# Kernel optimization log

Hardware: AMD Instinct MI355X
Metric: run time of the kernel (lower is better)

The kernel has to match this reference:

```python
import jax, jax.numpy as jnp
import numpy as np

TEMPERATURE = 0.1
MAX_POS = 6
MAX_NEG = 30
POS_NEG_RATIO = 1.0
NEG_K = max(6, MAX_NEG)  # static top-k width for negatives


def setup_inputs() -> dict:
    key = jax.random.key(0)
    k1, k2 = jax.random.split(key)
    K, D = 8192, 256
    features = jax.random.normal(k1, (K, D), dtype=jnp.float32)
    labels = jax.random.randint(k2, (K,), 0, 64, dtype=jnp.int64)
    return {"features": features, "labels": labels}


def reference(features, labels):
    K = features.shape[0]
    # L2-normalize embeddings (F.normalize, dim=1)
    f = features / jnp.clip(jnp.linalg.norm(features, axis=1, keepdims=True), 1e-12)
    sim = jnp.matmul(f, f.T) / TEMPERATURE                      # [K, K]
    sim = sim - jax.lax.stop_gradient(jnp.max(sim, axis=1, keepdims=True))
    exp_sim = jnp.exp(sim)

    eye = jnp.eye(K, dtype=bool)
    same = labels[:, None] == labels[None, :]
    mask_pos = same & ~eye                                      # same label, off-diagonal
    mask_neg = ~same                                            # 1 - mask_pos - eye

    n_pos = jnp.sum(mask_pos, axis=1).astype(jnp.int32)         # [K]
    n_neg = jnp.sum(mask_neg, axis=1).astype(jnp.int32)         # [K]

    # per-anchor dynamic sample counts (vectorized version of the python loop)
    max_pos_i = jnp.minimum(
        n_pos,
        jnp.maximum(1, jnp.minimum(MAX_POS, (n_neg.astype(jnp.float32) * POS_NEG_RATIO).astype(jnp.int32))),
    )
    max_neg_i = jnp.minimum(n_neg, NEG_K)
    valid_row = (n_pos > 0) & (n_neg > 0)
    max_pos_i = jnp.where(valid_row, max_pos_i, 0)
    max_neg_i = jnp.where(valid_row, max_neg_i, 0)

    rows = jnp.arange(K)[:, None]
    neg_inf = jnp.finfo(sim.dtype).min

    # top-k hard positives by similarity, masked to the first max_pos_i ranks
    pos_scores = jnp.where(mask_pos, sim, neg_inf)
    _, pos_idx = jax.lax.top_k(pos_scores, MAX_POS)             # [K, MAX_POS]
    pos_keep = (jnp.arange(MAX_POS)[None, :] < max_pos_i[:, None]).astype(sim.dtype)
    new_mask_pos = jnp.zeros((K, K), sim.dtype).at[rows, pos_idx].add(pos_keep)

    # random negatives: randperm emulated by top-k of uniform scores over neg slots
    rand = jax.random.uniform(jax.random.key(42), (K, K), dtype=jnp.float32)
    neg_scores = jnp.where(mask_neg, rand, -1.0)
    _, neg_idx = jax.lax.top_k(neg_scores, NEG_K)               # [K, NEG_K]
    neg_keep = (jnp.arange(NEG_K)[None, :] < max_neg_i[:, None]).astype(sim.dtype)
    new_mask_neg = jnp.zeros((K, K), sim.dtype).at[rows, neg_idx].add(neg_keep)

    numerator = jnp.sum(exp_sim * new_mask_pos, axis=1)
    denominator = jnp.sum(exp_sim * (new_mask_pos + new_mask_neg), axis=1)
    loss = -jnp.log(jnp.clip(numerator / denominator, 1e-8))
    return jnp.mean(loss)
```

## Files before the change

kernel.cpp:

```cpp
#include <hip/hip_runtime.h>
#include <hip/hip_fp16.h>
#include <math.h>
#include <stdint.h>


#define NEGK 30
#define MAXP 6
#define MAXBC 320
#define RGB 32
#define CGB 64

typedef _Float16 h2v __attribute__((ext_vector_type(2)));

__device__ __forceinline__ uint64_t mix64(uint64_t z) {
  z += 0x9E3779B97F4A7C15ULL;
  z = (z ^ (z >> 30)) * 0xBF58476D1CE4E5B9ULL;
  z = (z ^ (z >> 27)) * 0x94D049BB133111EBULL;
  return z ^ (z >> 31);
}

__device__ __forceinline__ float wave_reduce_add(float p) {
#pragma unroll
  for (int o = 32; o; o >>= 1) p += __shfl_down(p, o, 64);
  return p;
}

__device__ __forceinline__ float dot8h(uint4 a, uint4 b, float acc) {
  const h2v* pa = (const h2v*)&a;
  const h2v* pb = (const h2v*)&b;
#if __has_builtin(__builtin_amdgcn_fdot2)
#pragma unroll
  for (int q = 0; q < 4; ++q) acc = __builtin_amdgcn_fdot2(pa[q], pb[q], acc, false);
#else
#pragma unroll
  for (int q = 0; q < 4; ++q)
    acc += (float)pa[q].x * (float)pb[q].x + (float)pa[q].y * (float)pb[q].y;
#endif
  return acc;
}

__global__ __launch_bounds__(256) void k_prep(const float* __restrict__ F,
                                              const int* __restrict__ labels, int K,
                                              __half* __restrict__ Fh,
                                              int* __restrict__ g_start,
                                              int* __restrict__ g_soff,
                                              int* __restrict__ g_bucket,
                                              int4* __restrict__ g_meta) {
  __shared__ int cnt[64], start[65], cur[64], soff_s[64];
  const int tid = threadIdx.x;

  if ((int)blockIdx.x < K / 4) {
    const int row = blockIdx.x * 4 + (tid >> 6);
    const int lane = tid & 63;
    const float4 a = ((const float4*)(F + (size_t)row * 256))[lane];
    float p = a.x * a.x + a.y * a.y + a.z * a.z + a.w * a.w;
    p = wave_reduce_add(p);
    p = __shfl(p, 0, 64);
    const float inv = 1.0f / fmaxf(sqrtf(p), 1e-12f);
    union { __half2 h[2]; uint2 u; } cv;
    cv.h[0] = __float22half2_rn(make_float2(a.x * inv, a.y * inv));
    cv.h[1] = __float22half2_rn(make_float2(a.z * inv, a.w * inv));
    ((uint2*)(Fh + (size_t)row * 256))[lane] = cv.u;
    return;
  }

  if (tid < 64) cnt[tid] = 0;
  __syncthreads();
  for (int t = tid; t < K; t += 256) atomicAdd(&cnt[labels[t] & 63], 1);
  __syncthreads();
  if (tid == 0) {
    int acc = 0, sacc = 0;
    for (int l = 0; l < 64; ++l) {
      start[l] = acc;
      const int B = cnt[l];
      acc += B;
      soff_s[l] = sacc;
      const int Bc = B < MAXBC ? B : MAXBC;
      sacc += Bc * Bc;
    }
    start[64] = acc;
  }
  __syncthreads();
  if (tid < 64) { cur[tid] = start[tid]; g_soff[tid] = soff_s[tid]; }
  if (tid < 65) g_start[tid] = start[tid];
  __syncthreads();
  for (int t = tid; t < K; t += 256) {
    const int l = labels[t] & 63;
    const int p = atomicAdd(&cur[l], 1);
    g_bucket[p] = t;
    g_meta[t] = make_int4(start[l], cnt[l], p - start[l], soff_s[l]);
  }
}

__global__ __launch_bounds__(256) void k_gram(const __half* __restrict__ Fh,
                                              const int* __restrict__ g_start,
                                              const int* __restrict__ g_soff,
                                              const int* __restrict__ g_bucket,
                                              float* __restrict__ g_sims) {
  __shared__ uint4 sA[RGB * 32];

  const int b  = blockIdx.x;
  const int bs = g_start[b];
  const int B  = g_start[b + 1] - bs;
  const int Bc = B < MAXBC ? B : MAXBC;
  const int r0 = blockIdx.y * RGB;
  const int c0 = blockIdx.z * CGB;
  if (r0 >= Bc || c0 >= Bc) return;
  const int tid = threadIdx.x;

  for (int u = tid; u < RGB * 32; u += 256) {
    const int r = u >> 5, c = u & 31;
    const int rr = r0 + r;
    const int gr = g_bucket[bs + (rr < Bc ? rr : Bc - 1)];
    sA[u] = ((const uint4*)(Fh + (size_t)gr * 256))[c];
  }
  __syncthreads();

  const int wv = tid >> 6, lane = tid & 63;
  const int cc = c0 + lane;
  const int gq = g_bucket[bs + (cc < Bc ? cc : Bc - 1)];
  const uint4* fq = (const uint4*)(Fh + (size_t)gq * 256);
  const uint4* sw = sA + wv * 8 * 32;

  float acc[8];
#pragma unroll
  for (int r = 0; r < 8; ++r) acc[r] = 0.0f;

  for (int k = 0; k < 32; k += 4) {
    const uint4 a0 = fq[k], a1 = fq[k + 1], a2 = fq[k + 2], a3 = fq[k + 3];
#pragma unroll
    for (int r = 0; r < 8; ++r) {
      float t = acc[r];
      t = dot8h(sw[r * 32 + k    ], a0, t);
      t = dot8h(sw[r * 32 + k + 1], a1, t);
      t = dot8h(sw[r * 32 + k + 2], a2, t);
      t = dot8h(sw[r * 32 + k + 3], a3, t);
      acc[r] = t;
    }
  }

  if (cc < Bc) {
    float* outb = g_sims + g_soff[b];
#pragma unroll
    for (int r = 0; r < 8; ++r) {
      const int rr = r0 + wv * 8 + r;
      if (rr < Bc)
        outb[(size_t)rr * Bc + cc] = (rr == cc) ? -3.0e38f : acc[r] * 10.0f;
    }
  }
}

__global__ __launch_bounds__(256) void k_anchor(
    const __half* __restrict__ Fh, const int* __restrict__ g_bucket,
    const int4* __restrict__ g_meta, const float* __restrict__ g_sims,
    float* __restrict__ g_part, int K) {
  const int wv = threadIdx.x >> 6;
  const int lane = threadIdx.x & 63;
  const int i = blockIdx.x * 4 + wv;

  const int4 mt = g_meta[i];
  const int bs = mt.x, B = mt.y;
  const int Bc = B < MAXBC ? B : MAXBC;
  int loc = mt.z;
  if (loc >= Bc) loc = 0;
  const int n_pos = B - 1;
  const int n_neg = K - B;
  const float* simrow = g_sims + mt.w + (size_t)loc * Bc;

  const int s = lane & 3, g = lane >> 2;
  const uint4* fi4 = (const uint4*)(Fh + (size_t)i * 256);
  uint4 fi[8];
#pragma unroll
  for (int k = 0; k < 8; ++k) fi[k] = fi4[k * 4 + s];

  float v[5];
#pragma unroll
  for (int rr = 0; rr < 5; ++rr) {
    const int t = lane + rr * 64;
    v[rr] = (t < Bc) ? simrow[t] : -3.4e38f;
  }

  int t6 = n_neg < MAXP ? n_neg : MAXP;
  if (t6 < 1) t6 = 1;
  int take = n_pos < t6 ? n_pos : t6;
  if (n_pos <= 0 || n_neg <= 0) take = 0;

  float num = 0.0f;
  for (int r = 0; r < take; ++r) {
    float best = -3.4e38f;
    int bi = 0x7FFFFFFF;
#pragma unroll
    for (int rr = 0; rr < 5; ++rr) {
      if (v[rr] > best) { best = v[rr]; bi = rr * 64 + lane; }
    }
#pragma unroll
    for (int o = 1; o < 64; o <<= 1) {
      const float ov = __shfl_xor(best, o, 64);
      const int oi = __shfl_xor(bi, o, 64);
      if (ov > best || (ov == best && oi < bi)) { best = ov; bi = oi; }
    }
    num += expf(best);
    const int rsel = bi >> 6;
    if ((bi & 63) == lane) {
#pragma unroll
      for (int rr = 0; rr < 5; ++rr)
        if (rr == rsel) v[rr] = -3.4e38f;
    }
  }

  const int target = (take > 0) ? (n_neg < NEGK ? n_neg : NEGK) : 0;
  unsigned int rdraw = 0x40000000u + lane;
  if (lane < target) {
    const uint64_t z = mix64(((uint64_t)(uint32_t)i << 32) | (uint32_t)lane);
    rdraw = (unsigned int)(((uint64_t)(uint32_t)z * (uint64_t)n_neg) >> 32);
  }
  for (int round = 0; round < 8; ++round) {
    bool dup = false;
    for (int l2 = 0; l2 < NEGK; ++l2) {
      const unsigned int vv = __shfl(rdraw, l2, 64);
      if (l2 < lane && vv == rdraw) dup = true;
    }
    if (!__any(dup)) break;
    if (dup && lane < target) {
      const uint64_t z =
          mix64(((uint64_t)(uint32_t)i << 32) | (uint32_t)(lane + 64 * (round + 1)));
      rdraw = (unsigned int)(((uint64_t)(uint32_t)z * (uint64_t)n_neg) >> 32);
    }
  }
  int myj = 0;
  if (lane < target) {
    const int pos = (rdraw < (unsigned int)bs) ? (int)rdraw : (int)rdraw + B;
    myj = g_bucket[pos];
  }

  float e = 0.0f;
#pragma unroll
  for (int r = 0; r < 2; ++r) {
    const int t = r * 16 + g;
    const int j = __shfl(myj, t, 64);
    const uint4* fj = (const uint4*)(Fh + (size_t)j * 256);
    float d = 0.0f;
#pragma unroll
    for (int k = 0; k < 8; ++k) d = dot8h(fj[k * 4 + s], fi[k], d);
    d += __shfl_xor(d, 1, 64);
    d += __shfl_xor(d, 2, 64);
    if (s == 0 && t < target) e += expf(d * 10.0f);
  }
  const float wsum = wave_reduce_add(e);

  if (lane == 0) {
    const float denom = num + wsum;
    float ratio = denom > 0.0f ? num / denom : 0.0f;
    ratio = fmaxf(ratio, 1e-8f);
    g_part[i] = -logf(ratio);
  }
}

__global__ __launch_bounds__(1024) void k_final(const float* __restrict__ g_part,
                                                float* __restrict__ out, int K) {
  __shared__ float s[16];
  float p = 0.0f;
  for (int t = threadIdx.x; t < K; t += 1024) p += g_part[t];
  p = wave_reduce_add(p);
  if ((threadIdx.x & 63) == 0) s[threadIdx.x >> 6] = p;
  __syncthreads();
  if (threadIdx.x == 0) {
    float tot = 0.0f;
#pragma unroll
    for (int w = 0; w < 16; ++w) tot += s[w];
    out[0] = tot / (float)K;
  }
}

extern "C" void kernel_launch(void* const* d_in, const int* in_sizes, int n_in,
                              void* d_out, int out_size, void* d_ws, size_t ws_size,
                              hipStream_t stream) {
  (void)n_in; (void)out_size; (void)ws_size;
  const float* F = (const float*)d_in[0];
  const int* labels = (const int*)d_in[1];
  const int K = in_sizes[1];
  float* out = (float*)d_out;

  char* ws = (char*)d_ws;
  size_t off = 0;
  int*   g_start  = (int*)(ws + off);   off += 512;
  int*   g_soff   = (int*)(ws + off);   off += 256;
  int*   g_bucket = (int*)(ws + off);   off += (size_t)K * 4;
  float* g_part   = (float*)(ws + off); off += (size_t)K * 4;
  off = (off + 255) & ~(size_t)255;
  int4*  g_meta   = (int4*)(ws + off);  off += (size_t)K * 16;
  __half* Fh      = (__half*)(ws + off); off += (size_t)K * 256 * 2;
  float* g_sims   = (float*)(ws + off);  off += (size_t)MAXBC * K * 4;

  k_prep<<<K / 4 + 1, 256, 0, stream>>>(F, labels, K, Fh, g_start, g_soff,
                                        g_bucket, g_meta);
  {
    dim3 grid(64, (MAXBC + RGB - 1) / RGB, (MAXBC + CGB - 1) / CGB);
    k_gram<<<grid, 256, 0, stream>>>(Fh, g_start, g_soff, g_bucket, g_sims);
  }
  k_anchor<<<K / 4, 256, 0, stream>>>(Fh, g_bucket, g_meta, g_sims, g_part, K);
  k_final<<<1, 1024, 0, stream>>>(g_part, out, K);
}
```

Measured before the change: 121.8 us.

## Fuse gram and anchor kernels, keep similarity tiles in registers

Merges the per-label gram kernel and the per-anchor loss kernel into one kernel, so each block computes a 32-anchor by full-bucket similarity tile in registers and does the positive top-k selection and negative sampling directly. This removes the global similarity buffer write and read-back and one kernel launch. The duplicate-rejection loop for negative draws is dropped, so repeated negative indices are no longer resampled. Parallelism drops to 64x10 blocks, each doing the whole row sweep, which risks lower occupancy and more serial work per block.

Measured after the change: 149.9 us. 23.0% more time.

```diff
diff --git a/kernel.cpp b/kernel.cpp
--- a/kernel.cpp
+++ b/kernel.cpp
@@ -7,8 +7,8 @@
 #define NEGK 30
 #define MAXP 6
 #define MAXBC 320
-#define RGB 32
-#define CGB 64
+#define RGM 32
+#define GRIDY ((MAXBC + RGM - 1) / RGM)
 
 typedef _Float16 h2v __attribute__((ext_vector_type(2)));
 
@@ -43,10 +43,8 @@
                                               const int* __restrict__ labels, int K,
                                               __half* __restrict__ Fh,
                                               int* __restrict__ g_start,
-                                              int* __restrict__ g_soff,
-                                              int* __restrict__ g_bucket,
-                                              int4* __restrict__ g_meta) {
-  __shared__ int cnt[64], start[65], cur[64], soff_s[64];
+                                              int* __restrict__ g_bucket) {
+  __shared__ int cnt[64], start[65], cur[64];
   const int tid = threadIdx.x;
 
   if ((int)blockIdx.x < K / 4) {
@@ -69,207 +67,179 @@
   for (int t = tid; t < K; t += 256) atomicAdd(&cnt[labels[t] & 63], 1);
   __syncthreads();
   if (tid == 0) {
-    int acc = 0, sacc = 0;
-    for (int l = 0; l < 64; ++l) {
-      start[l] = acc;
-      const int B = cnt[l];
-      acc += B;
-      soff_s[l] = sacc;
-      const int Bc = B < MAXBC ? B : MAXBC;
-      sacc += Bc * Bc;
-    }
+    int acc = 0;
+    for (int l = 0; l < 64; ++l) { start[l] = acc; acc += cnt[l]; }
     start[64] = acc;
   }
   __syncthreads();
-  if (tid < 64) { cur[tid] = start[tid]; g_soff[tid] = soff_s[tid]; }
+  if (tid < 64) cur[tid] = start[tid];
   if (tid < 65) g_start[tid] = start[tid];
   __syncthreads();
   for (int t = tid; t < K; t += 256) {
     const int l = labels[t] & 63;
     const int p = atomicAdd(&cur[l], 1);
     g_bucket[p] = t;
-    g_meta[t] = make_int4(start[l], cnt[l], p - start[l], soff_s[l]);
-  }
-}
-
-__global__ __launch_bounds__(256) void k_gram(const __half* __restrict__ Fh,
-                                              const int* __restrict__ g_start,
-                                              const int* __restrict__ g_soff,
-                                              const int* __restrict__ g_bucket,
-                                              float* __restrict__ g_sims) {
-  __shared__ uint4 sA[RGB * 32];
+  }
+}
+
+__global__ __launch_bounds__(256) void k_main(
+    const __half* __restrict__ Fh, const int* __restrict__ g_start,
+    const int* __restrict__ g_bucket, float* __restrict__ g_part, int K) {
+  __shared__ uint4 sAnch[RGM * 32];
+  __shared__ int   s_gid[RGM];
+  __shared__ float s_wsum[RGM];
+  __shared__ float s_loss[4];
 
   const int b  = blockIdx.x;
+  const int rg = blockIdx.y;
+  const int bid = b * GRIDY + rg;
   const int bs = g_start[b];
   const int B  = g_start[b + 1] - bs;
   const int Bc = B < MAXBC ? B : MAXBC;
-  const int r0 = blockIdx.y * RGB;
-  const int c0 = blockIdx.z * CGB;
-  if (r0 >= Bc || c0 >= Bc) return;
+  const int p0 = rg * RGM;
   const int tid = threadIdx.x;
-
-  for (int u = tid; u < RGB * 32; u += 256) {
-    const int r = u >> 5, c = u & 31;
-    const int rr = r0 + r;
-    const int gr = g_bucket[bs + (rr < Bc ? rr : Bc - 1)];
-    sA[u] = ((const uint4*)(Fh + (size_t)gr * 256))[c];
-  }
-  __syncthreads();
+  if (p0 >= Bc) { if (tid == 0) g_part[bid] = 0.0f; return; }
 
   const int wv = tid >> 6, lane = tid & 63;
-  const int cc = c0 + lane;
-  const int gq = g_bucket[bs + (cc < Bc ? cc : Bc - 1)];
-  const uint4* fq = (const uint4*)(Fh + (size_t)gq * 256);
-  const uint4* sw = sA + wv * 8 * 32;
-
-  float acc[8];
-#pragma unroll
-  for (int r = 0; r < 8; ++r) acc[r] = 0.0f;
-
-  for (int k = 0; k < 32; k += 4) {
-    const uint4 a0 = fq[k], a1 = fq[k + 1], a2 = fq[k + 2], a3 = fq[k + 3];
-#pragma unroll
-    for (int r = 0; r < 8; ++r) {
-      float t = acc[r];
-      t = dot8h(sw[r * 32 + k    ], a0, t);
-      t = dot8h(sw[r * 32 + k + 1], a1, t);
-      t = dot8h(sw[r * 32 + k + 2], a2, t);
-      t = dot8h(sw[r * 32 + k + 3], a3, t);
-      acc[r] = t;
-    }
-  }
-
-  if (cc < Bc) {
-    float* outb = g_sims + g_soff[b];
-#pragma unroll
-    for (int r = 0; r < 8; ++r) {
-      const int rr = r0 + wv * 8 + r;
-      if (rr < Bc)
-        outb[(size_t)rr * Bc + cc] = (rr == cc) ? -3.0e38f : acc[r] * 10.0f;
-    }
-  }
-}
-
-__global__ __launch_bounds__(256) void k_anchor(
-    const __half* __restrict__ Fh, const int* __restrict__ g_bucket,
-    const int4* __restrict__ g_meta, const float* __restrict__ g_sims,
-    float* __restrict__ g_part, int K) {
-  const int wv = threadIdx.x >> 6;
-  const int lane = threadIdx.x & 63;
-  const int i = blockIdx.x * 4 + wv;
-
-  const int4 mt = g_meta[i];
-  const int bs = mt.x, B = mt.y;
-  const int Bc = B < MAXBC ? B : MAXBC;
-  int loc = mt.z;
-  if (loc >= Bc) loc = 0;
   const int n_pos = B - 1;
   const int n_neg = K - B;
-  const float* simrow = g_sims + mt.w + (size_t)loc * Bc;
-
-  const int s = lane & 3, g = lane >> 2;
-  const uint4* fi4 = (const uint4*)(Fh + (size_t)i * 256);
-  uint4 fi[8];
-#pragma unroll
-  for (int k = 0; k < 8; ++k) fi[k] = fi4[k * 4 + s];
-
-  float v[5];
-#pragma unroll
-  for (int rr = 0; rr < 5; ++rr) {
-    const int t = lane + rr * 64;
-    v[rr] = (t < Bc) ? simrow[t] : -3.4e38f;
+
+  for (int u = tid; u < RGM * 32; u += 256) {
+    const int r = u >> 5, c = u & 31;
+    const int p = p0 + r;
+    const int gr = g_bucket[bs + (p < Bc ? p : Bc - 1)];
+    sAnch[u] = ((const uint4*)(Fh + (size_t)gr * 256))[c];
+  }
+  if (tid < RGM) {
+    const int p = p0 + tid;
+    s_gid[tid] = (p < Bc) ? g_bucket[bs + p] : 0;
+    s_wsum[tid] = 0.0f;
+  }
+  __syncthreads();
+
+  const uint4* sw = sAnch + (wv * 8) * 32;
+
+  float v[5][8];
+#pragma unroll
+  for (int c = 0; c < 5; ++c)
+#pragma unroll
+    for (int r = 0; r < 8; ++r) v[c][r] = -3.4e38f;
+
+#pragma unroll
+  for (int c = 0; c < 5; ++c) {
+    if (c * 64 < Bc) {
+      const int cc = c * 64 + lane;
+      const int gq = g_bucket[bs + (cc < Bc ? cc : Bc - 1)];
+      const uint4* fq = (const uint4*)(Fh + (size_t)gq * 256);
+      float acc[8];
+#pragma unroll
+      for (int r = 0; r < 8; ++r) acc[r] = 0.0f;
+      for (int k = 0; k < 32; k += 4) {
+        const uint4 a0 = fq[k], a1 = fq[k + 1], a2 = fq[k + 2], a3 = fq[k + 3];
+#pragma unroll
+        for (int r = 0; r < 8; ++r) {
+          float t = acc[r];
+          t = dot8h(sw[r * 32 + k    ], a0, t);
+          t = dot8h(sw[r * 32 + k + 1], a1, t);
+          t = dot8h(sw[r * 32 + k + 2], a2, t);
+          t = dot8h(sw[r * 32 + k + 3], a3, t);
+          acc[r] = t;
+        }
+      }
+      if (cc < Bc) {
+#pragma unroll
+        for (int r = 0; r < 8; ++r) {
+          const int p = p0 + wv * 8 + r;
+          v[c][r] = (cc == p) ? -3.0e38f : acc[r] * 10.0f;
+        }
+      }
+    }
   }
 
   int t6 = n_neg < MAXP ? n_neg : MAXP;
   if (t6 < 1) t6 = 1;
   int take = n_pos < t6 ? n_pos : t6;
   if (n_pos <= 0 || n_neg <= 0) take = 0;
-
-  float num = 0.0f;
-  for (int r = 0; r < take; ++r) {
-    float best = -3.4e38f;
-    int bi = 0x7FFFFFFF;
-#pragma unroll
-    for (int rr = 0; rr < 5; ++rr) {
-      if (v[rr] > best) { best = v[rr]; bi = rr * 64 + lane; }
+  const int target = (take > 0) ? (n_neg < NEGK ? n_neg : NEGK) : 0;
+
+  float num[8];
+#pragma unroll
+  for (int r = 0; r < 8; ++r) {
+    float nm = 0.0f;
+    for (int t = 0; t < take; ++t) {
+      float best = -3.4e38f;
+      int bi = 0x7FFFFFFF;
+#pragma unroll
+      for (int c = 0; c < 5; ++c) {
+        if (v[c][r] > best) { best = v[c][r]; bi = c * 64 + lane; }
+      }
+#pragma unroll
+      for (int o = 1; o < 64; o <<= 1) {
+        const float ov = __shfl_xor(best, o, 64);
+        const int oi = __shfl_xor(bi, o, 64);
+        if (ov > best || (ov == best && oi < bi)) { best = ov; bi = oi; }
+      }
+      nm += expf(best);
+      const int csel = bi >> 6;
+      if ((bi & 63) == lane) {
+#pragma unroll
+        for (int c = 0; c < 5; ++c)
+          if (c == csel) v[c][r] = -3.4e38f;
+      }
     }
-#pragma unroll
-    for (int o = 1; o < 64; o <<= 1) {
-      const float ov = __shfl_xor(best, o, 64);
-      const int oi = __shfl_xor(bi, o, 64);
-      if (ov > best || (ov == best && oi < bi)) { best = ov; bi = oi; }
-    }
-    num += expf(best);
-    const int rsel = bi >> 6;
-    if ((bi & 63) == lane) {
-#pragma unroll
-      for (int rr = 0; rr < 5; ++rr)
-        if (rr == rsel) v[rr] = -3.4e38f;
-    }
-  }
-
-  const int target = (take > 0) ? (n_neg < NEGK ? n_neg : NEGK) : 0;
-  unsigned int rdraw = 0x40000000u + lane;
-  if (lane < target) {
-    const uint64_t z = mix64(((uint64_t)(uint32_t)i << 32) | (uint32_t)lane);
-    rdraw = (unsigned int)(((uint64_t)(uint32_t)z * (uint64_t)n_neg) >> 32);
-  }
-  for (int round = 0; round < 8; ++round) {
-    bool dup = false;
-    for (int l2 = 0; l2 < NEGK; ++l2) {
-      const unsigned int vv = __shfl(rdraw, l2, 64);
-      if (l2 < lane && vv == rdraw) dup = true;
-    }
-    if (!__any(dup)) break;
-    if (dup && lane < target) {
-      const uint64_t z =
-          mix64(((uint64_t)(uint32_t)i << 32) | (uint32_t)(lane + 64 * (round + 1)));
-      rdraw = (unsigned int)(((uint64_t)(uint32_t)z * (uint64_t)n_neg) >> 32);
-    }
-  }
-  int myj = 0;
-  if (lane < target) {
+    num[r] = nm;
+  }
+
+  const int s = lane & 3, g = lane >> 2;
+  for (int t = 0; t < (8 * NEGK) / 16; ++t) {
+    const int pair = t * 16 + g;
+    const int a = pair / NEGK, n = pair % NEGK;
+    const int p = p0 + wv * 8 + a;
+    const bool pv = (p < Bc) && (n < target);
+    const int ig = s_gid[wv * 8 + a];
+    const uint64_t z = mix64(((uint64_t)(uint32_t)ig << 32) | (uint32_t)n);
+    const unsigned int rdraw =
+        (unsigned int)(((uint64_t)(uint32_t)z * (uint64_t)n_neg) >> 32);
     const int pos = (rdraw < (unsigned int)bs) ? (int)rdraw : (int)rdraw + B;
-    myj = g_bucket[pos];
-  }
-
-  float e = 0.0f;
-#pragma unroll
-  for (int r = 0; r < 2; ++r) {
-    const int t = r * 16 + g;
-    const int j = __shfl(myj, t, 64);
+    const int j = pv ? g_bucket[pos] : 0;
     const uint4* fj = (const uint4*)(Fh + (size_t)j * 256);
     float d = 0.0f;
 #pragma unroll
-    for (int k = 0; k < 8; ++k) d = dot8h(fj[k * 4 + s], fi[k], d);
+    for (int k = 0; k < 8; ++k)
+      d = dot8h(fj[k * 4 + s], sAnch[(wv * 8 + a) * 32 + k * 4 + s], d);
     d += __shfl_xor(d, 1, 64);
     d += __shfl_xor(d, 2, 64);
-    if (s == 0 && t < target) e += expf(d * 10.0f);
-  }
-  const float wsum = wave_reduce_add(e);
+    if (s == 0 && pv) atomicAdd(&s_wsum[wv * 8 + a], expf(d * 10.0f));
+  }
+  __syncthreads();
 
   if (lane == 0) {
-    const float denom = num + wsum;
-    float ratio = denom > 0.0f ? num / denom : 0.0f;
-    ratio = fmaxf(ratio, 1e-8f);
-    g_part[i] = -logf(ratio);
-  }
-}
-
-__global__ __launch_bounds__(1024) void k_final(const float* __restrict__ g_part,
-                                                float* __restrict__ out, int K) {
-  __shared__ float s[16];
+    float ls = 0.0f;
+#pragma unroll
+    for (int r = 0; r < 8; ++r) {
+      const int p = p0 + wv * 8 + r;
+      if (p < Bc && take > 0) {
+        const float denom = num[r] + s_wsum[wv * 8 + r];
+        float ratio = denom > 0.0f ? num[r] / denom : 0.0f;
+        ratio = fmaxf(ratio, 1e-8f);
+        ls += -logf(ratio);
+      }
+    }
+    s_loss[wv] = ls;
+  }
+  __syncthreads();
+  if (tid == 0) g_part[bid] = s_loss[0] + s_loss[1] + s_loss[2] + s_loss[3];
+}
+
+__global__ __launch_bounds__(256) void k_final(const float* __restrict__ g_part,
+                                               float* __restrict__ out, int K) {
+  __shared__ float s[4];
   float p = 0.0f;
-  for (int t = threadIdx.x; t < K; t += 1024) p += g_part[t];
+  for (int t = threadIdx.x; t < 64 * GRIDY; t += 256) p += g_part[t];
   p = wave_reduce_add(p);
   if ((threadIdx.x & 63) == 0) s[threadIdx.x >> 6] = p;
   __syncthreads();
-  if (threadIdx.x == 0) {
-    float tot = 0.0f;
-#pragma unroll
-    for (int w = 0; w < 16; ++w) tot += s[w];
-    out[0] = tot / (float)K;
-  }
+  if (threadIdx.x == 0) out[0] = (s[0] + s[1] + s[2] + s[3]) / (float)K;
 }
 
 extern "C" void kernel_launch(void* const* d_in, const int* in_sizes, int n_in,
@@ -284,20 +254,15 @@
   char* ws = (char*)d_ws;
   size_t off = 0;
   int*   g_start  = (int*)(ws + off);   off += 512;
-  int*   g_soff   = (int*)(ws + off);   off += 256;
   int*   g_bucket = (int*)(ws + off);   off += (size_t)K * 4;
-  float* g_part   = (float*)(ws + off); off += (size_t)K * 4;
+  float* g_part   = (float*)(ws + off); off += (size_t)64 * GRIDY * 4;
   off = (off + 255) & ~(size_t)255;
-  int4*  g_meta   = (int4*)(ws + off);  off += (size_t)K * 16;
   __half* Fh      = (__half*)(ws + off); off += (size_t)K * 256 * 2;
-  float* g_sims   = (float*)(ws + off);  off += (size_t)MAXBC * K * 4;
-
-  k_prep<<<K / 4 + 1, 256, 0, stream>>>(F, labels, K, Fh, g_start, g_soff,
-                                        g_bucket, g_meta);
+
+  k_prep<<<K / 4 + 1, 256, 0, stream>>>(F, labels, K, Fh, g_start, g_bucket);
   {
-    dim3 grid(64, (MAXBC + RGB - 1) / RGB, (MAXBC + CGB - 1) / CGB);
-    k_gram<<<grid, 256, 0, stream>>>(Fh, g_start, g_soff, g_bucket, g_sims);
-  }
-  k_anchor<<<K / 4, 256, 0, stream>>>(Fh, g_bucket, g_meta, g_sims, g_part, K);
-  k_final<<<1, 1024, 0, stream>>>(g_part, out, K);
-}
+    dim3 grid(64, GRIDY, 1);
+    k_main<<<grid, 256, 0, stream>>>(Fh, g_start, g_bucket, g_part, K);
+  }
+  k_final<<<1, 256, 0, stream>>>(g_part, out, K);
+}
```
